# Kernel tuning notes

Measured on AMD Instinct MI355X. Metric: run time of the kernel, lower is better.

Reference implementation:

```python
import jax, jax.numpy as jnp
from jax import lax
import numpy as np
import math

B, W, C, H, K = 4, 1024, 1024, 16, 3  # batch, frames(cropsize), bins, num_bands, kernel
D = C // H  # head dim


def setup_inputs() -> dict:
    key = jax.random.key(0)
    ks = jax.random.split(key, 17)
    lin = lambda k: jax.random.normal(k, (C, C), jnp.float32) * 0.02
    vec = lambda k: jax.random.normal(k, (C,), jnp.float32) * 0.02
    cw = lambda k: jax.random.normal(k, (C, 1, K), jnp.float32) * 0.2  # depthwise conv weight (O, I/g=1, K)
    return {
        'x': jax.random.normal(ks[0], (B, W, C), jnp.float32),
        'qW': lin(ks[1]), 'qb': vec(ks[2]), 'qcw': cw(ks[3]), 'qcb': vec(ks[4]),
        'kW': lin(ks[5]), 'kb': vec(ks[6]), 'kcw': cw(ks[7]), 'kcb': vec(ks[8]),
        'vW': lin(ks[9]), 'vb': vec(ks[10]), 'vcw': cw(ks[11]), 'vcb': vec(ks[12]),
        'oW': lin(ks[13]), 'ob': vec(ks[14]),
        'er': jax.random.normal(ks[15], (D, W), jnp.float32),
    }


def _causal_dwconv(x_bwc, w, b):
    # x: (B, W, C) -> conv over time with left pad K-1, depthwise (groups=C)
    y = lax.conv_general_dilated(
        x_bwc.transpose(0, 2, 1), w, window_strides=(1,), padding=[(K - 1, 0)],
        feature_group_count=C, dimension_numbers=('NCH', 'OIH', 'NCH'))
    return (y + b[None, :, None]).transpose(0, 2, 1)


def reference(x, qW, qb, qcw, qcb, kW, kb, kcw, kcb, vW, vb, vcw, vcb, oW, ob, er):
    q = _causal_dwconv(x @ qW.T + qb, qcw, qcb).reshape(B, W, H, D).transpose(0, 2, 1, 3)  # bhwd
    k = _causal_dwconv(x @ kW.T + kb, kcw, kcb).reshape(B, W, H, D).transpose(0, 2, 3, 1)  # bhdw
    v = _causal_dwconv(x @ vW.T + vb, vcw, vcb).reshape(B, W, H, D).transpose(0, 2, 1, 3)  # bhwd
    # Music-Transformer relative position skewing
    p = jnp.pad(jnp.einsum('bhwd,dt->bhwt', q, er), ((0, 0), (0, 0), (0, 0), (1, 0)))
    p = p.transpose(0, 1, 3, 2)[:, :, 1:, :]  # (B,H,W,W)
    qk = (jnp.matmul(q, k) + p) / math.sqrt(C)
    a = jax.nn.softmax(qk, axis=-1)
    o = jnp.matmul(a, v).transpose(0, 2, 1, 3).reshape(B, W, C)
    return o @ oW.T + ob
```

## Files before the change

### kernel.cpp

```cpp
#include <hip/hip_runtime.h>

#define B_ 4
#define W_ 1024
#define C_ 1024
#define H_ 16
#define D_ 64

typedef __attribute__((ext_vector_type(8))) short short8;
typedef __attribute__((ext_vector_type(4))) float f32x4;

__device__ __forceinline__ unsigned short f2b(float f) {
  unsigned u = __builtin_bit_cast(unsigned, f);
  unsigned r = (u + 0x7fffu + ((u >> 16) & 1u)) >> 16;
  return (unsigned short)r;
}
__device__ __forceinline__ float b2f(short b) {
  return __builtin_bit_cast(float, ((unsigned)(unsigned short)b) << 16);
}
__device__ __forceinline__ unsigned pk2(float a, float b) {
  unsigned r;
  asm("v_cvt_pk_bf16_f32 %0, %1, %2" : "=v"(r) : "v"(a), "v"(b));
  return r;
}

typedef __attribute__((address_space(1))) void GV;
typedef __attribute__((address_space(3))) void LV;
__device__ __forceinline__ void gl16(const short* g, short* l) {
  __builtin_amdgcn_global_load_lds((GV*)g, (LV*)l, 16, 0, 0);
}

__global__ __launch_bounds__(256)
void prep_kernel(const float* __restrict__ x, const float* __restrict__ qW,
                 const float* __restrict__ kW, const float* __restrict__ vW,
                 const float* __restrict__ oW, const float* __restrict__ er,
                 short* __restrict__ xh, short* __restrict__ wh,
                 short* __restrict__ ertb) {
  const int bx = blockIdx.x;
  const int tid = threadIdx.x;
  if (bx < 4096) {
    const float* s;
    short* d;
    size_t u;
    if (bx < 2048) {
      u = (size_t)bx * 256 + tid;
      s = x; d = xh;
    } else {
      u = (size_t)(bx - 2048) * 256 + tid;
      const int w = (int)(u >> 17);
      s = (w == 0) ? qW : (w == 1) ? kW : (w == 2) ? vW : oW;
      d = wh + (u & ~(size_t)131071) * 8;
      u &= 131071;
      const float4* p = (const float4*)s + u * 2;
      float4 a = p[0], b = p[1];
      short8 r;
      r[0] = f2b(a.x); r[1] = f2b(a.y); r[2] = f2b(a.z); r[3] = f2b(a.w);
      r[4] = f2b(b.x); r[5] = f2b(b.y); r[6] = f2b(b.z); r[7] = f2b(b.w);
      *((short8*)d + u) = r;
      return;
    }
    const float4* p = (const float4*)s + u * 2;
    float4 a = p[0], b = p[1];
    short8 r;
    r[0] = f2b(a.x); r[1] = f2b(a.y); r[2] = f2b(a.z); r[3] = f2b(a.w);
    r[4] = f2b(b.x); r[5] = f2b(b.y); r[6] = f2b(b.z); r[7] = f2b(b.w);
    *((short8*)d + u) = r;
  } else {
    int i = (bx - 4096) * 256 + tid;
    int d = i >> 8;
    int w4 = (i & 255) << 2;
    float4 v = *(const float4*)(er + (size_t)d * W_ + w4);
    ertb[(size_t)(w4 + 0) * D_ + d] = f2b(v.x);
    ertb[(size_t)(w4 + 1) * D_ + d] = f2b(v.y);
    ertb[(size_t)(w4 + 2) * D_ + d] = f2b(v.z);
    ertb[(size_t)(w4 + 3) * D_ + d] = f2b(v.w);
  }
}

template <int OUTF32>
__global__ __launch_bounds__(256)
void gemm_bf16_v2(const short* __restrict__ A, const short* __restrict__ Wt,
                  const float* __restrict__ b0, const float* __restrict__ b1,
                  const float* __restrict__ b2, void* __restrict__ outv,
                  int M, int N, int K) {
  __shared__ short sA[128 * 64];
  __shared__ short sB[128 * 64];
  const int tid = threadIdx.x;
  const int bm = blockIdx.y * 128, bn = blockIdx.x * 128;
  const int wv = tid >> 6, lane = tid & 63;
  const int wr = (wv >> 1) * 64, wc = (wv & 1) * 64;
  const int l15 = lane & 15, l4 = lane >> 4;
  const int srow = tid >> 3;
  const int scs = (tid & 7) * 8;
  const short* ga = A + (size_t)(bm + srow) * K + scs;
  const short* gb = Wt + (size_t)(bn + srow) * K + scs;
  short* la = sA + tid * 8;
  short* lb = sB + tid * 8;

  f32x4 acc[4][4];
#pragma unroll
  for (int mf = 0; mf < 4; ++mf)
#pragma unroll
    for (int nf = 0; nf < 4; ++nf) acc[mf][nf] = (f32x4){0.f, 0.f, 0.f, 0.f};

  for (int k0 = 0; k0 < K; k0 += 64) {
    __syncthreads();
#pragma unroll
    for (int i = 0; i < 4; ++i) {
      gl16(ga + (size_t)(i * 32) * K + k0, la + i * 2048);
      gl16(gb + (size_t)(i * 32) * K + k0, lb + i * 2048);
    }
    __syncthreads();
#pragma unroll
    for (int ks = 0; ks < 2; ++ks) {
      short8 af[4], bf[4];
#pragma unroll
      for (int mf = 0; mf < 4; ++mf)
        af[mf] = *(short8*)(sA + (wr + mf * 16 + l15) * 64 + ks * 32 + l4 * 8);
#pragma unroll
      for (int nf = 0; nf < 4; ++nf)
        bf[nf] = *(short8*)(sB + (wc + nf * 16 + l15) * 64 + ks * 32 + l4 * 8);
#pragma unroll
      for (int mf = 0; mf < 4; ++mf)
#pragma unroll
        for (int nf = 0; nf < 4; ++nf)
          acc[mf][nf] = __builtin_amdgcn_mfma_f32_16x16x32_bf16(af[mf], bf[nf], acc[mf][nf], 0, 0, 0);
    }
  }
#pragma unroll
  for (int mf = 0; mf < 4; ++mf) {
#pragma unroll
    for (int nf = 0; nf < 4; ++nf) {
      const int n = bn + wc + nf * 16 + l15;
      const float bs = (n < 1024) ? b0[n] : ((n < 2048) ? b1[n - 1024] : b2[n - 2048]);
#pragma unroll
      for (int r = 0; r < 4; ++r) {
        const int m = bm + wr + mf * 16 + l4 * 4 + r;
        const float v = acc[mf][nf][r] + bs;
        if (OUTF32) ((float*)outv)[(size_t)m * N + n] = v;
        else        ((short*)outv)[(size_t)m * N + n] = (short)f2b(v);
      }
    }
  }
}

__global__ __launch_bounds__(256)
void dwconv_qk_kernel(const short* __restrict__ yqkv,
                      const float* __restrict__ qcw, const float* __restrict__ qcb,
                      const float* __restrict__ kcw, const float* __restrict__ kcb,
                      short* __restrict__ qc, short* __restrict__ kc) {
  const int t = blockIdx.y;
  const float* cw = t ? kcw : qcw;
  const float* cb = t ? kcb : qcb;
  short* out = t ? kc : qc;
  const int idx = blockIdx.x * 256 + threadIdx.x;
  const int c8 = (idx & (C_ / 8 - 1)) << 3;
  const int bw = idx >> 7;
  const int w = bw & (W_ - 1);
  const short* base = yqkv + (size_t)bw * (3 * C_) + t * C_ + c8;
  short8 x2 = *(const short8*)base;
  short8 x1, x0;
  if (w >= 1) x1 = *(const short8*)(base - 3 * C_); else { for (int j = 0; j < 8; ++j) x1[j] = 0; }
  if (w >= 2) x0 = *(const short8*)(base - 6 * C_); else { for (int j = 0; j < 8; ++j) x0[j] = 0; }
  short8 r;
#pragma unroll
  for (int j = 0; j < 8; ++j) {
    const int c = c8 + j;
    float acc = b2f(x0[j]) * cw[c * 3 + 0] + b2f(x1[j]) * cw[c * 3 + 1] +
                b2f(x2[j]) * cw[c * 3 + 2] + cb[c];
    r[j] = (short)f2b(acc);
  }
  *(short8*)(out + (size_t)bw * C_ + c8) = r;
}

__global__ __launch_bounds__(256)
void dwconv_vt_kernel(const short* __restrict__ yqkv, const float* __restrict__ vcw,
                      const float* __restrict__ vcb, short* __restrict__ vt) {
  __shared__ short t[64][72];
  const int bh = blockIdx.y, w0 = blockIdx.x * 64;
  const int b = bh >> 4, h = bh & 15;
  const int tid = threadIdx.x;
  for (int c = tid; c < 512; c += 256) {
    const int w = c >> 3, dg = c & 7;
    const int gw = w0 + w;
    const short* base = yqkv + ((size_t)(b * W_ + gw)) * (3 * C_) + 2 * C_ + h * 64 + dg * 8;
    short8 x2 = *(const short8*)base;
    short8 x1, x0;
    if (gw >= 1) x1 = *(const short8*)(base - 3 * C_); else { for (int j = 0; j < 8; ++j) x1[j] = 0; }
    if (gw >= 2) x0 = *(const short8*)(base - 6 * C_); else { for (int j = 0; j < 8; ++j) x0[j] = 0; }
#pragma unroll
    for (int j = 0; j < 8; ++j) {
      const int ch = h * 64 + dg * 8 + j;
      float acc = b2f(x0[j]) * vcw[ch * 3 + 0] + b2f(x1[j]) * vcw[ch * 3 + 1] +
                  b2f(x2[j]) * vcw[ch * 3 + 2] + vcb[ch];
      t[dg * 8 + j][w] = (short)f2b(acc);
    }
  }
  __syncthreads();
  for (int c = tid; c < 512; c += 256) {
    const int d = c >> 3, wg = c & 7;
    *(short8*)(vt + ((size_t)(bh * 64 + d)) * W_ + w0 + wg * 8) = *(short8*)&t[d][wg * 8];
  }
}

__global__ __launch_bounds__(256)
void attn_v3_kernel(const short* __restrict__ q, const short* __restrict__ k,
                    const short* __restrict__ vt, const short* __restrict__ ert,
                    short* __restrict__ o) {
  __shared__ short sK[2][4096];
  __shared__ short sQj[2][4096];
  __shared__ short sVt[2][4096];
  __shared__ short sU[8192];
  short* sQ = sU;
  short* sE = sU + 4096;
  short* sP = sU;

  const int tid = threadIdx.x;
  const int wid = blockIdx.x;
  const int swz = (wid & 7) * 128 + (wid >> 3);
  const int bh = swz >> 4, qt = swz & 15;
  const int b = bh >> 4, h = bh & 15;
  const int i0 = qt * 64;
  const int wv = tid >> 6, lane = tid & 63;
  const int l15 = lane & 15, l4 = lane >> 4;
  const size_t bW = (size_t)b * W_;
  const int srow = tid >> 3;
  const int swsc = ((tid & 7) ^ (srow & 7)) * 8;
  const int cxor = (l15 & 7) * 8;

  const short* qbase = q + bW * C_ + h * 64;
  const short* kbase = k + bW * C_ + h * 64;
  const short* vbase = vt + (size_t)bh * 64 * W_;

  {
    const short* g;
    g = qbase + (size_t)(i0 + srow) * C_ + swsc;
    gl16(g, sQ + tid * 8); gl16(g + (size_t)32 * C_, sQ + 2048 + tid * 8);
    g = ert + (size_t)(i0 + srow) * 64 + swsc;
    gl16(g, sE + tid * 8); gl16(g + 32 * 64, sE + 2048 + tid * 8);
    g = kbase + (size_t)srow * C_ + swsc;
    gl16(g, sK[0] + tid * 8); gl16(g + (size_t)32 * C_, sK[0] + 2048 + tid * 8);
    g = qbase + (size_t)srow * C_ + swsc;
    gl16(g, sQj[0] + tid * 8); gl16(g + (size_t)32 * C_, sQj[0] + 2048 + tid * 8);
    g = vbase + (size_t)srow * W_ + swsc;
    gl16(g, sVt[0] + tid * 8); gl16(g + (size_t)32 * W_, sVt[0] + 2048 + tid * 8);
  }
  __syncthreads();

  short8 bQ[2], bE[2];
#pragma unroll
  for (int ks = 0; ks < 2; ++ks) {
    const int off = (ks * 32 + l4 * 8) ^ cxor;
    bQ[ks] = *(short8*)(sQ + (wv * 16 + l15) * 64 + off);
    bE[ks] = *(short8*)(sE + (wv * 16 + l15) * 64 + off);
  }
  __syncthreads();

  float m_ = -1e30f, l_ = 0.f;
  f32x4 accO[4];
#pragma unroll
  for (int mf = 0; mf < 4; ++mf) accO[mf] = (f32x4){0.f, 0.f, 0.f, 0.f};
  const float SC = 0.03125f;

  for (int jt = 0; jt < 16; ++jt) {
    const int cur = jt & 1;
    if (jt < 15) {
      const int j0n = (jt + 1) * 64;
      const short* g;
      g = kbase + (size_t)(j0n + srow) * C_ + swsc;
      gl16(g, sK[cur ^ 1] + tid * 8); gl16(g + (size_t)32 * C_, sK[cur ^ 1] + 2048 + tid * 8);
      g = qbase + (size_t)(j0n + srow) * C_ + swsc;
      gl16(g, sQj[cur ^ 1] + tid * 8); gl16(g + (size_t)32 * C_, sQj[cur ^ 1] + 2048 + tid * 8);
      g = vbase + (size_t)srow * W_ + j0n + swsc;
      gl16(g, sVt[cur ^ 1] + tid * 8); gl16(g + (size_t)32 * W_, sVt[cur ^ 1] + 2048 + tid * 8);
    }

    f32x4 s[4];
#pragma unroll
    for (int mf = 0; mf < 4; ++mf) s[mf] = (f32x4){0.f, 0.f, 0.f, 0.f};
    const int ofA = (l4 * 8) ^ cxor;
    const int ofB = (32 + l4 * 8) ^ cxor;
    __builtin_amdgcn_s_setprio(1);
#pragma unroll
    for (int mf = 0; mf < 4; ++mf) {
      const short* kp = sK[cur] + (mf * 16 + l15) * 64;
      const short* jp = sQj[cur] + (mf * 16 + l15) * 64;
      s[mf] = __builtin_amdgcn_mfma_f32_16x16x32_bf16(*(short8*)(kp + ofA), bQ[0], s[mf], 0, 0, 0);
      s[mf] = __builtin_amdgcn_mfma_f32_16x16x32_bf16(*(short8*)(kp + ofB), bQ[1], s[mf], 0, 0, 0);
      s[mf] = __builtin_amdgcn_mfma_f32_16x16x32_bf16(*(short8*)(jp + ofA), bE[0], s[mf], 0, 0, 0);
      s[mf] = __builtin_amdgcn_mfma_f32_16x16x32_bf16(*(short8*)(jp + ofB), bE[1], s[mf], 0, 0, 0);
    }
    __builtin_amdgcn_s_setprio(0);

    float px = fmaxf(fmaxf(s[0][0], s[0][1]), fmaxf(s[0][2], s[0][3]));
#pragma unroll
    for (int mf = 1; mf < 4; ++mf)
      px = fmaxf(px, fmaxf(fmaxf(s[mf][0], s[mf][1]), fmaxf(s[mf][2], s[mf][3])));
    px = fmaxf(px, __shfl_xor(px, 16));
    px = fmaxf(px, __shfl_xor(px, 32));
    px *= SC;
    if (!__all(px <= m_ + 8.f)) {
      const float mn = fmaxf(m_, px);
      const float sc = __expf(m_ - mn);
      l_ *= sc;
#pragma unroll
      for (int mf = 0; mf < 4; ++mf)
#pragma unroll
        for (int r = 0; r < 4; ++r) accO[mf][r] *= sc;
      m_ = mn;
    }
    float p[4][4];
    float rs = 0.f;
#pragma unroll
    for (int mf = 0; mf < 4; ++mf)
#pragma unroll
      for (int r = 0; r < 4; ++r) {
        p[mf][r] = __expf(__builtin_fmaf(s[mf][r], SC, -m_));
        rs += p[mf][r];
      }
    rs += __shfl_xor(rs, 16);
    rs += __shfl_xor(rs, 32);
    l_ += rs;

#pragma unroll
    for (int mf = 0; mf < 4; ++mf) {
      uint2 w2;
      w2.x = pk2(p[mf][0], p[mf][1]);
      w2.y = pk2(p[mf][2], p[mf][3]);
      const int off = (((2 * mf + (l4 >> 1)) ^ (l15 & 7)) * 8) + (l4 & 1) * 4;
      *(uint2*)(sP + (wv * 16 + l15) * 64 + off) = w2;
    }

    short8 pf[2];
#pragma unroll
    for (int ks = 0; ks < 2; ++ks)
      pf[ks] = *(short8*)(sP + (wv * 16 + l15) * 64 + ((ks * 32 + l4 * 8) ^ cxor));
    __builtin_amdgcn_s_setprio(1);
#pragma unroll
    for (int mf = 0; mf < 4; ++mf) {
      const short* vp = sVt[cur] + (mf * 16 + l15) * 64;
      accO[mf] = __builtin_amdgcn_mfma_f32_16x16x32_bf16(*(short8*)(vp + ofA), pf[0], accO[mf], 0, 0, 0);
      accO[mf] = __builtin_amdgcn_mfma_f32_16x16x32_bf16(*(short8*)(vp + ofB), pf[1], accO[mf], 0, 0, 0);
    }
    __builtin_amdgcn_s_setprio(0);

    __syncthreads();
  }

  const float inv = 1.f / l_;
  const size_t orow = (bW + i0 + wv * 16 + l15) * C_ + h * 64;
#pragma unroll
  for (int mf = 0; mf < 4; ++mf) {
    uint2 w2;
    w2.x = pk2(accO[mf][0] * inv, accO[mf][1] * inv);
    w2.y = pk2(accO[mf][2] * inv, accO[mf][3] * inv);
    *(uint2*)(o + orow + mf * 16 + l4 * 4) = w2;
  }
}

extern "C" void kernel_launch(void* const* d_in, const int* in_sizes, int n_in,
                              void* d_out, int out_size, void* d_ws, size_t ws_size,
                              hipStream_t stream) {
  (void)in_sizes; (void)n_in; (void)out_size; (void)ws_size;
  const float* x   = (const float*)d_in[0];
  const float* qW  = (const float*)d_in[1];
  const float* qb  = (const float*)d_in[2];
  const float* qcw = (const float*)d_in[3];
  const float* qcb = (const float*)d_in[4];
  const float* kW  = (const float*)d_in[5];
  const float* kb  = (const float*)d_in[6];
  const float* kcw = (const float*)d_in[7];
  const float* kcb = (const float*)d_in[8];
  const float* vW  = (const float*)d_in[9];
  const float* vb  = (const float*)d_in[10];
  const float* vcw = (const float*)d_in[11];
  const float* vcb = (const float*)d_in[12];
  const float* oW  = (const float*)d_in[13];
  const float* ob  = (const float*)d_in[14];
  const float* er  = (const float*)d_in[15];
  float* out = (float*)d_out;

  const size_t NE = (size_t)B_ * W_ * C_;
  const size_t NW = (size_t)C_ * C_;
  short* ws   = (short*)d_ws;
  short* xh    = ws;
  short* wqkvh = xh + NE;
  short* oWh   = wqkvh + 3 * NW;
  short* ertb  = oWh + NW;
  short* yqkv  = ertb + (size_t)W_ * D_;
  short* qc    = yqkv + (size_t)(B_ * W_) * (3 * C_);
  short* kc    = qc + NE;
  short* vt    = xh;
  short* oat   = yqkv;

  prep_kernel<<<4160, 256, 0, stream>>>(x, qW, kW, vW, oW, er, xh, wqkvh, ertb);

  const int M = B_ * W_;
  dim3 gq(3 * C_ / 128, M / 128);
  gemm_bf16_v2<0><<<gq, 256, 0, stream>>>(xh, wqkvh, qb, kb, vb, yqkv, M, 3 * C_, C_);

  dwconv_qk_kernel<<<dim3(2048, 2), 256, 0, stream>>>(yqkv, qcw, qcb, kcw, kcb, qc, kc);
  dwconv_vt_kernel<<<dim3(W_ / 64, B_ * H_), 256, 0, stream>>>(yqkv, vcw, vcb, vt);

  attn_v3_kernel<<<1024, 256, 0, stream>>>(qc, kc, vt, ertb, oat);

  dim3 go(C_ / 128, M / 128);
  gemm_bf16_v2<1><<<go, 256, 0, stream>>>(oat, oWh, ob, ob, ob, out, M, C_, C_);
}
```

Baseline: 258.7 us.

## Double-buffer GEMM LDS tiles and XOR-swizzle columns to avoid bank conflicts

```diff
diff --git a/kernel.cpp b/kernel.cpp
--- a/kernel.cpp
+++ b/kernel.cpp
@@ -76,25 +76,38 @@
   }
 }
 
+#define GSTAGE(T, BUF)                                                       \
+  {                                                                          \
+    const int k0_ = (T) * 64;                                                \
+    gl16(ga + (size_t)0  * K + k0_, sA[BUF] + 0    + ldst);                  \
+    gl16(gb + (size_t)0  * K + k0_, sB[BUF] + 0    + ldst);                  \
+    gl16(ga + (size_t)32 * K + k0_, sA[BUF] + 2048 + ldst);                  \
+    gl16(gb + (size_t)32 * K + k0_, sB[BUF] + 2048 + ldst);                  \
+    gl16(ga + (size_t)64 * K + k0_, sA[BUF] + 4096 + ldst);                  \
+    gl16(gb + (size_t)64 * K + k0_, sB[BUF] + 4096 + ldst);                  \
+    gl16(ga + (size_t)96 * K + k0_, sA[BUF] + 6144 + ldst);                  \
+    gl16(gb + (size_t)96 * K + k0_, sB[BUF] + 6144 + ldst);                  \
+  }
+
 template <int OUTF32>
 __global__ __launch_bounds__(256)
-void gemm_bf16_v2(const short* __restrict__ A, const short* __restrict__ Wt,
+void gemm_bf16_v3(const short* __restrict__ A, const short* __restrict__ Wt,
                   const float* __restrict__ b0, const float* __restrict__ b1,
                   const float* __restrict__ b2, void* __restrict__ outv,
                   int M, int N, int K) {
-  __shared__ short sA[128 * 64];
-  __shared__ short sB[128 * 64];
+  __shared__ short sA[2][128 * 64];
+  __shared__ short sB[2][128 * 64];
   const int tid = threadIdx.x;
   const int bm = blockIdx.y * 128, bn = blockIdx.x * 128;
   const int wv = tid >> 6, lane = tid & 63;
   const int wr = (wv >> 1) * 64, wc = (wv & 1) * 64;
   const int l15 = lane & 15, l4 = lane >> 4;
   const int srow = tid >> 3;
-  const int scs = (tid & 7) * 8;
-  const short* ga = A + (size_t)(bm + srow) * K + scs;
-  const short* gb = Wt + (size_t)(bn + srow) * K + scs;
-  short* la = sA + tid * 8;
-  short* lb = sB + tid * 8;
+  const int swsc = ((tid & 7) ^ (srow & 7)) * 8;
+  const int cxor = (l15 & 7) * 8;
+  const int ldst = tid * 8;
+  const short* ga = A + (size_t)(bm + srow) * K + swsc;
+  const short* gb = Wt + (size_t)(bn + srow) * K + swsc;
 
   f32x4 acc[4][4];
 #pragma unroll
@@ -102,29 +115,35 @@
 #pragma unroll
     for (int nf = 0; nf < 4; ++nf) acc[mf][nf] = (f32x4){0.f, 0.f, 0.f, 0.f};
 
-  for (int k0 = 0; k0 < K; k0 += 64) {
-    __syncthreads();
-#pragma unroll
-    for (int i = 0; i < 4; ++i) {
-      gl16(ga + (size_t)(i * 32) * K + k0, la + i * 2048);
-      gl16(gb + (size_t)(i * 32) * K + k0, lb + i * 2048);
-    }
-    __syncthreads();
+  const int nt = K >> 6;
+  GSTAGE(0, 0)
+  for (int t = 0; t < nt; ++t) {
+    const int cur = t & 1;
+    if (t + 1 < nt) {
+      GSTAGE(t + 1, cur ^ 1)
+      asm volatile("s_waitcnt vmcnt(8)" ::: "memory");
+    } else {
+      asm volatile("s_waitcnt vmcnt(0)" ::: "memory");
+    }
+    __builtin_amdgcn_s_barrier();
+    __builtin_amdgcn_sched_barrier(0);
 #pragma unroll
     for (int ks = 0; ks < 2; ++ks) {
       short8 af[4], bf[4];
 #pragma unroll
       for (int mf = 0; mf < 4; ++mf)
-        af[mf] = *(short8*)(sA + (wr + mf * 16 + l15) * 64 + ks * 32 + l4 * 8);
+        af[mf] = *(short8*)(sA[cur] + (wr + mf * 16 + l15) * 64 + ((ks * 32 + l4 * 8) ^ cxor));
 #pragma unroll
       for (int nf = 0; nf < 4; ++nf)
-        bf[nf] = *(short8*)(sB + (wc + nf * 16 + l15) * 64 + ks * 32 + l4 * 8);
+        bf[nf] = *(short8*)(sB[cur] + (wc + nf * 16 + l15) * 64 + ((ks * 32 + l4 * 8) ^ cxor));
 #pragma unroll
       for (int mf = 0; mf < 4; ++mf)
 #pragma unroll
         for (int nf = 0; nf < 4; ++nf)
           acc[mf][nf] = __builtin_amdgcn_mfma_f32_16x16x32_bf16(af[mf], bf[nf], acc[mf][nf], 0, 0, 0);
     }
+    __builtin_amdgcn_sched_barrier(0);
+    __builtin_amdgcn_s_barrier();
   }
 #pragma unroll
   for (int mf = 0; mf < 4; ++mf) {
@@ -396,7 +415,7 @@
 
   const int M = B_ * W_;
   dim3 gq(3 * C_ / 128, M / 128);
-  gemm_bf16_v2<0><<<gq, 256, 0, stream>>>(xh, wqkvh, qb, kb, vb, yqkv, M, 3 * C_, C_);
+  gemm_bf16_v3<0><<<gq, 256, 0, stream>>>(xh, wqkvh, qb, kb, vb, yqkv, M, 3 * C_, C_);
 
   dwconv_qk_kernel<<<dim3(2048, 2), 256, 0, stream>>>(yqkv, qcw, qcb, kcw, kcb, qc, kc);
   dwconv_vt_kernel<<<dim3(W_ / 64, B_ * H_), 256, 0, stream>>>(yqkv, vcw, vcb, vt);
@@ -404,5 +423,5 @@
   attn_v3_kernel<<<1024, 256, 0, stream>>>(qc, kc, vt, ertb, oat);
 
   dim3 go(C_ / 128, M / 128);
-  gemm_bf16_v2<1><<<go, 256, 0, stream>>>(oat, oWh, ob, ob, ob, out, M, C_, C_);
-}
+  gemm_bf16_v3<1><<<go, 256, 0, stream>>>(oat, oWh, ob, ob, ob, out, M, C_, C_);
+}
```

Result: faster. 242.3 us (-6.3%).
